# Kernel tuning notes

Measured on AMD Instinct MI355X. Metric: run time of the kernel, lower is better.

## Reference

```python
import jax, jax.numpy as jnp
import numpy as np

HEADS = 4

def gat_layer(x, W, a_src, a_dst, bias, edge_index, n):
    # PyG-style GATConv with self-loops, heads averaged (concat=False) so out dim == hidden_dim
    H, C = a_src.shape
    h = (x @ W).reshape(n, H, C)                      # [N,H,C]
    loops = jnp.arange(n)
    src = jnp.concatenate([edge_index[0], loops])
    dst = jnp.concatenate([edge_index[1], loops])
    e = jax.nn.leaky_relu((h * a_src).sum(-1)[src] + (h * a_dst).sum(-1)[dst], 0.2)  # [E,H]
    m = jax.ops.segment_max(e, dst, num_segments=n)   # segment softmax over incoming edges
    ex = jnp.exp(e - m[dst])
    s = jax.ops.segment_sum(ex, dst, num_segments=n)
    alpha = ex / (s[dst] + 1e-16)
    out = jax.ops.segment_sum(alpha[:, :, None] * h[src], dst, num_segments=n)  # [N,H,C]
    return out.mean(axis=1) + bias

def setup_inputs() -> dict:
    key = jax.random.key(0)
    ks = jax.random.split(key, 24)
    Nd, Ni, Ne = 20000, 4096, 4096
    D_in, D = 512, 256
    n_int, n_emo = 64, 32
    inp = {}
    inp['dialogue_embeddings'] = jax.random.normal(ks[0], (Nd, D_in), jnp.float32)
    inp['intention_indices'] = jax.random.randint(ks[1], (Ni,), 0, n_int)
    inp['emotion_indices'] = jax.random.randint(ks[2], (Ne,), 0, n_emo)
    inp['dialogue_edge_index'] = jax.random.randint(ks[3], (2, Nd * 32), 0, Nd)
    inp['intention_edge_index'] = jax.random.randint(ks[4], (2, Ni * 16), 0, Ni)
    inp['emotion_edge_index'] = jax.random.randint(ks[5], (2, Ne * 16), 0, Ne)
    s = lambda k, shape: jax.random.normal(k, shape, jnp.float32) * 0.02
    inp['intention_emb'] = s(ks[6], (n_int, D))
    inp['emotion_emb'] = s(ks[7], (n_emo, D))
    inp['Wd'] = s(ks[8], (D_in, HEADS * D)); inp['a_src_d'] = s(ks[9], (HEADS, D)); inp['a_dst_d'] = s(ks[10], (HEADS, D)); inp['bd'] = jnp.zeros((D,), jnp.float32)
    inp['Wi'] = s(ks[11], (D, HEADS * D)); inp['a_src_i'] = s(ks[12], (HEADS, D)); inp['a_dst_i'] = s(ks[13], (HEADS, D)); inp['bi'] = jnp.zeros((D,), jnp.float32)
    inp['We'] = s(ks[14], (D, HEADS * D)); inp['a_src_e'] = s(ks[15], (HEADS, D)); inp['a_dst_e'] = s(ks[16], (HEADS, D)); inp['be'] = jnp.zeros((D,), jnp.float32)
    inp['W_dfc'] = s(ks[17], (D, D)); inp['b_dfc'] = jnp.zeros((D,), jnp.float32)
    inp['W_ifc'] = s(ks[18], (D, D)); inp['b_ifc'] = jnp.zeros((D,), jnp.float32)
    inp['W_efc'] = s(ks[19], (D, D)); inp['b_efc'] = jnp.zeros((D,), jnp.float32)
    inp['W_fc'] = s(ks[20], (3 * D, n_emo)); inp['b_fc'] = jnp.zeros((n_emo,), jnp.float32)
    return inp

def reference(dialogue_embeddings, intention_indices, emotion_indices,
              dialogue_edge_index, intention_edge_index, emotion_edge_index,
              intention_emb, emotion_emb,
              Wd, a_src_d, a_dst_d, bd, Wi, a_src_i, a_dst_i, bi,
              We, a_src_e, a_dst_e, be,
              W_dfc, b_dfc, W_ifc, b_ifc, W_efc, b_efc, W_fc, b_fc):
    Nd = dialogue_embeddings.shape[0]
    Ni = intention_indices.shape[0]
    Ne = emotion_indices.shape[0]
    ie = intention_emb[intention_indices]   # [Ni, D]
    ee = emotion_emb[emotion_indices]       # [Ne, D]
    d = gat_layer(dialogue_embeddings, Wd, a_src_d, a_dst_d, bd, dialogue_edge_index, Nd)
    d = jax.nn.relu(d @ W_dfc + b_dfc)
    i = gat_layer(ie, Wi, a_src_i, a_dst_i, bi, intention_edge_index, Ni)
    i = jax.nn.relu(i @ W_ifc + b_ifc)
    e = gat_layer(ee, We, a_src_e, a_dst_e, be, emotion_edge_index, Ne)
    e = jax.nn.relu(e @ W_efc + b_efc)
    iw = jax.nn.softmax(d @ i.T, axis=-1)   # [Nd, Ni]
    att_i = iw @ i                           # [Nd, D]
    ew = jax.nn.softmax(d @ e.T, axis=-1)   # [Nd, Ne]
    att_e = ew @ e                           # [Nd, D]
    inputs = jnp.concatenate([d, att_i, att_e], axis=-1)  # [Nd, 3D]
    return inputs @ W_fc + b_fc
```

## Files before the change

### kernel.cpp

```cpp
#include <hip/hip_runtime.h>
#include <hip/hip_bf16.h>
#include <math.h>

#define DEV static __device__ __forceinline__

typedef __attribute__((ext_vector_type(8))) short short8;
typedef __attribute__((ext_vector_type(4))) short short4v;
typedef __attribute__((ext_vector_type(4))) float f32x4;
typedef __attribute__((ext_vector_type(2))) long long2v;

DEV float bf2f(__hip_bfloat16 x) { return __bfloat162float(x); }
DEV __hip_bfloat16 f2bf(float x) { return __float2bfloat16(x); }
DEV short bfbits(float x) { __hip_bfloat16 h = __float2bfloat16(x); short s; __builtin_memcpy(&s, &h, 2); return s; }
DEV float b2f_bits(short s) { __hip_bfloat16 h; __builtin_memcpy(&h, &s, 2); return __bfloat162float(h); }
DEV float lrelu(float x) { return x > 0.f ? x : 0.2f * x; }

DEV float load_in(const void* p, long long i, bool f32) {
  return f32 ? ((const float*)p)[i] : bf2f(((const __hip_bfloat16*)p)[i]);
}

DEV long pack8_fp8(const float* f) {
  int lo = 0, hi = 0;
  lo = __builtin_amdgcn_cvt_pk_fp8_f32(f[0], f[1], lo, false);
  lo = __builtin_amdgcn_cvt_pk_fp8_f32(f[2], f[3], lo, true);
  hi = __builtin_amdgcn_cvt_pk_fp8_f32(f[4], f[5], hi, false);
  hi = __builtin_amdgcn_cvt_pk_fp8_f32(f[6], f[7], hi, true);
  return ((long)(unsigned)hi << 32) | (unsigned)lo;
}

DEV f32x4 mfma_fp8(long a, long b, f32x4 c) {
  return __builtin_amdgcn_mfma_f32_16x16x32_fp8_fp8(a, b, c, 0, 0, 0);
}

__global__ void HGAN_45148696215914_kernel() {}

__global__ void fill_k(__hip_bfloat16* __restrict__ p, float v, int n)
{
  int i = blockIdx.x * blockDim.x + threadIdx.x;
  if (i < n) p[i] = __float2bfloat16(v);
}

struct DetectArgs { const unsigned int* p[23]; int nw[23]; int id[23]; };

__global__ void detect_k(DetectArgs a, int* __restrict__ flags)
{
  __shared__ int cnt_sh;
  if (threadIdx.x == 0) cnt_sh = 0;
  __syncthreads();
  const unsigned int* w = a.p[blockIdx.x];
  int nwords = a.nw[blockIdx.x];
  int bad = 0;
  for (int i = threadIdx.x; i < nwords; i += blockDim.x) {
    unsigned int x = w[i];
    float v0 = __uint_as_float((x & 0xffffu) << 16);
    float v1 = __uint_as_float(x & 0xffff0000u);
    if (!(fabsf(v0) <= 1e4f)) bad++;
    if (!(fabsf(v1) <= 1e4f)) bad++;
  }
  atomicAdd(&cnt_sh, bad);
  __syncthreads();
  if (threadIdx.x == 0) flags[a.id[blockIdx.x]] = (cnt_sh > nwords / 4) ? 1 : 0;
}

struct CvArgs {
  const void* in[7]; const int* flag[7]; __hip_bfloat16* out[7];
  int K[7], N[7], NL[7], toff[7]; int nseg;
};

__global__ __launch_bounds__(256) void convtrN_k(CvArgs a)
{
  __shared__ __hip_bfloat16 t[32][33];
  int b = blockIdx.x;
  int s = 0;
  while (s + 1 < a.nseg && b >= a.toff[s + 1]) ++s;
  int ti = b - a.toff[s];
  int kb = a.K[s] >> 5;
  int bk = ti % kb, bn = ti / kb;
  const void* in = a.in[s];
  const int* flag = a.flag[s];
  __hip_bfloat16* out = a.out[s];
  int K = a.K[s], N = a.N[s];
  const bool f = flag && *flag;
  int lx = threadIdx.x & 31, ly = threadIdx.x >> 5;
  int gn = bn * 32 + lx;
#pragma unroll
  for (int rr = 0; rr < 32; rr += 8)
    t[rr + ly][lx] = (gn < N)
        ? f2bf(load_in(in, (long long)(bk * 32 + rr + ly) * N + gn, f))
        : f2bf(0.f);
  __syncthreads();
#pragma unroll
  for (int rr = 0; rr < 32; rr += 8)
    out[(size_t)(bn * 32 + rr + ly) * K + bk * 32 + lx] = t[lx][rr + ly];
}

DEV void mgemm_body(
    const void* A, const int* aflag, int lda, const int* idxA,
    const __hip_bfloat16* BT, void* C, int ldc,
    const void* bias, const int* biasflag, int relu,
    int permC, int M, int K, int Nlim, const int* cflag,
    int m0, int n0, __hip_bfloat16* Ash, __hip_bfloat16* Bsh)
{
  const bool af = aflag && *aflag;
  const bool bsf = biasflag && *biasflag;
  const bool cf = cflag && *cflag;
  const int tid = threadIdx.x;
  const int wv = tid >> 6, lane = tid & 63, qd = lane >> 4, lm = lane & 15;
  const int wr = wv >> 1, wc = wv & 1;

  f32x4 acc[4][4];
#pragma unroll
  for (int i = 0; i < 4; ++i)
    for (int j = 0; j < 4; ++j)
      for (int v = 0; v < 4; ++v) acc[i][j][v] = 0.f;

  for (int k0 = 0; k0 < K; k0 += 64) {
    __syncthreads();
    for (int u = tid; u < 1024; u += 256) {
      int r = u >> 3, cu = u & 7;
      int gm = m0 + r;
      short8 vv;
      if (gm < M) {
        long long row = idxA ? idxA[gm] : gm;
        long long basei = row * (long long)lda + k0 + cu * 8;
        if (af) {
          const float4* fp = (const float4*)((const float*)A + basei);
          float4 f0 = fp[0], f1 = fp[1];
          vv[0] = bfbits(f0.x); vv[1] = bfbits(f0.y);
          vv[2] = bfbits(f0.z); vv[3] = bfbits(f0.w);
          vv[4] = bfbits(f1.x); vv[5] = bfbits(f1.y);
          vv[6] = bfbits(f1.z); vv[7] = bfbits(f1.w);
        } else {
          vv = *(const short8*)((const __hip_bfloat16*)A + basei);
        }
      } else {
#pragma unroll
        for (int j = 0; j < 8; ++j) vv[j] = 0;
      }
      *(short8*)(&Ash[r * 72 + cu * 8]) = vv;
    }
    for (int u = tid; u < 1024; u += 256) {
      int r = u >> 3, cu = u & 7;
      *(short8*)(&Bsh[r * 72 + cu * 8]) =
          *(const short8*)(BT + (size_t)(n0 + r) * K + k0 + cu * 8);
    }
    __syncthreads();
#pragma unroll
    for (int ks = 0; ks < 2; ++ks) {
      short8 a[4], b[4];
#pragma unroll
      for (int i = 0; i < 4; ++i)
        a[i] = *(const short8*)(&Ash[(wr * 64 + i * 16 + lm) * 72 + ks * 32 + qd * 8]);
#pragma unroll
      for (int j = 0; j < 4; ++j)
        b[j] = *(const short8*)(&Bsh[(wc * 64 + j * 16 + lm) * 72 + ks * 32 + qd * 8]);
#pragma unroll
      for (int i = 0; i < 4; ++i)
#pragma unroll
        for (int j = 0; j < 4; ++j)
          acc[i][j] = __builtin_amdgcn_mfma_f32_16x16x32_bf16(a[i], b[j], acc[i][j], 0, 0, 0);
    }
  }
#pragma unroll
  for (int j = 0; j < 4; ++j) {
    int gn = n0 + wc * 64 + j * 16 + lm;
    if (gn >= Nlim) continue;
    float bv = bias ? load_in(bias, gn, bsf) : 0.f;
    int gcol = permC ? ((gn & 255) * 4 + (gn >> 8)) : gn;
#pragma unroll
    for (int i = 0; i < 4; ++i) {
#pragma unroll
      for (int v = 0; v < 4; ++v) {
        int gm = m0 + wr * 64 + i * 16 + qd * 4 + v;
        if (gm >= M) continue;
        float x = acc[i][j][v] + bv;
        if (relu) x = fmaxf(x, 0.f);
        long long idx = (long long)gm * ldc + gcol;
        if (cf) ((float*)C)[idx] = x;
        else    ((__hip_bfloat16*)C)[idx] = f2bf(x);
      }
    }
  }
}

__global__ __launch_bounds__(256) void mgemm_k(
    const void* __restrict__ A, const int* __restrict__ aflag, int lda,
    const int* __restrict__ idxA,
    const __hip_bfloat16* __restrict__ BT,
    void* __restrict__ C, int ldc,
    const void* __restrict__ bias, const int* __restrict__ biasflag, int relu,
    int permC, int M, int N, int K, int Nlim,
    const int* __restrict__ cflag)
{
  __shared__ __align__(16) __hip_bfloat16 Ash[128 * 72];
  __shared__ __align__(16) __hip_bfloat16 Bsh[128 * 72];
  (void)N;
  mgemm_body(A, aflag, lda, idxA, BT, C, ldc, bias, biasflag, relu,
             permC, M, K, Nlim, cflag,
             blockIdx.y * 128, blockIdx.x * 128, Ash, Bsh);
}

struct SegArgs {
  const void* A[3]; const int* aflag[3]; int lda[3]; const int* idxA[3];
  const __hip_bfloat16* BT[3]; void* C[3]; int ldc[3];
  const void* bias[3]; const int* bflag[3];
  int M[3]; int K[3]; int yoff[3];
  int relu, permC, Nlim;
};

__global__ __launch_bounds__(256) void mgemm_seg_k(SegArgs a)
{
  __shared__ __align__(16) __hip_bfloat16 Ash[128 * 72];
  __shared__ __align__(16) __hip_bfloat16 Bsh[128 * 72];
  int y = blockIdx.y;
  int s = (y >= a.yoff[2]) ? 2 : ((y >= a.yoff[1]) ? 1 : 0);
  mgemm_body(a.A[s], a.aflag[s], a.lda[s], a.idxA[s], a.BT[s], a.C[s], a.ldc[s],
             a.bias[s], a.bflag[s], a.relu, a.permC, a.M[s], a.K[s], a.Nlim,
             nullptr, (y - a.yoff[s]) * 128, blockIdx.x * 128, Ash, Bsh);
}

__global__ __launch_bounds__(256) void score3_k(
    const __hip_bfloat16* __restrict__ hI,
    const void* as1, const void* ad1, const int* sf1, const int* df1,
    const void* as2, const void* ad2, const int* sf2, const int* df2,
    const void* as3, const void* ad3, const int* sf3, const int* df3,
    int s1, int s2,
    float* __restrict__ ss, float* __restrict__ ds,
    int* __restrict__ cnt, int N)
{
  __shared__ float red[4][8];
  int n = blockIdx.x, c = threadIdx.x;
  if (c == 0) cnt[n] = 0;
  const void* a_src; const void* a_dst; const int* sfp; const int* dfp;
  if (n < s1)      { a_src = as1; a_dst = ad1; sfp = sf1; dfp = df1; }
  else if (n < s2) { a_src = as2; a_dst = ad2; sfp = sf2; dfp = df2; }
  else             { a_src = as3; a_dst = ad3; sfp = sf3; dfp = df3; }
  const bool sf = sfp && *sfp;
  const bool df = dfp && *dfp;
  short4v hv = *(const short4v*)(hI + (size_t)n * 1024 + c * 4);
  float h0 = b2f_bits(hv[0]), h1 = b2f_bits(hv[1]);
  float h2 = b2f_bits(hv[2]), h3 = b2f_bits(hv[3]);
  float r0 = h0 * load_in(a_src, 0 * 256 + c, sf);
  float r1 = h1 * load_in(a_src, 1 * 256 + c, sf);
  float r2 = h2 * load_in(a_src, 2 * 256 + c, sf);
  float r3 = h3 * load_in(a_src, 3 * 256 + c, sf);
  float t0 = h0 * load_in(a_dst, 0 * 256 + c, df);
  float t1 = h1 * load_in(a_dst, 1 * 256 + c, df);
  float t2 = h2 * load_in(a_dst, 2 * 256 + c, df);
  float t3 = h3 * load_in(a_dst, 3 * 256 + c, df);
#pragma unroll
  for (int o = 32; o > 0; o >>= 1) {
    r0 += __shfl_down(r0, o); r1 += __shfl_down(r1, o);
    r2 += __shfl_down(r2, o); r3 += __shfl_down(r3, o);
    t0 += __shfl_down(t0, o); t1 += __shfl_down(t1, o);
    t2 += __shfl_down(t2, o); t3 += __shfl_down(t3, o);
  }
  int wv = c >> 6, lane = c & 63;
  if (lane == 0) {
    red[wv][0] = r0; red[wv][1] = r1; red[wv][2] = r2; red[wv][3] = r3;
    red[wv][4] = t0; red[wv][5] = t1; red[wv][6] = t2; red[wv][7] = t3;
  }
  __syncthreads();
  if (c < 8) {
    float s = red[0][c] + red[1][c] + red[2][c] + red[3][c];
    if (c < 4) ss[n * 4 + c] = s;
    else       ds[n * 4 + (c - 4)] = s;
  }
}

__global__ void count3_k(const int* __restrict__ d1, int E1,
                         const int* __restrict__ d2, int E2, int o2,
                         const int* __restrict__ d3, int E3, int o3,
                         int* __restrict__ cnt)
{
  int k = blockIdx.x * blockDim.x + threadIdx.x;
  if (k < E1) atomicAdd(&cnt[d1[k]], 1);
  else if (k < E1 + E2) atomicAdd(&cnt[d2[k - E1] + o2], 1);
  else if (k < E1 + E2 + E3) atomicAdd(&cnt[d3[k - E1 - E2] + o3], 1);
}

__global__ __launch_bounds__(1024) void scan1_k(
    const int* __restrict__ cnt, int* __restrict__ offp, int* __restrict__ bsum, int n)
{
  __shared__ int sh[1024];
  int idx = blockIdx.x * 1024 + (int)threadIdx.x;
  int v = (idx < n) ? cnt[idx] : 0;
  sh[threadIdx.x] = v;
  __syncthreads();
  for (int d = 1; d < 1024; d <<= 1) {
    int t = (threadIdx.x >= (unsigned)d) ? sh[threadIdx.x - d] : 0;
    __syncthreads();
    sh[threadIdx.x] += t;
    __syncthreads();
  }
  if (idx < n) offp[idx] = sh[threadIdx.x] - v;
  if (threadIdx.x == 1023) bsum[blockIdx.x] = sh[1023];
}

__global__ void scan3_k(int* __restrict__ offp, const int* __restrict__ bsum,
                        int* __restrict__ cur, int n, int nb)
{
  int i = blockIdx.x * blockDim.x + threadIdx.x;
  if (i < n) {
    int chunk = i >> 10;
    int pre = 0;
    for (int b = 0; b < chunk; ++b) pre += bsum[b];
    int v = offp[i] + pre;
    offp[i] = v;
    cur[i] = v;
    if (i == n - 1) {
      int tot = 0;
      for (int b = 0; b < nb; ++b) tot += bsum[b];
      offp[n] = tot;
    }
  }
}

__global__ void scatter3_k(const int* __restrict__ s1, const int* __restrict__ d1, int E1,
                           const int* __restrict__ s2, const int* __restrict__ d2, int E2, int o2,
                           const int* __restrict__ s3, const int* __restrict__ d3, int E3, int o3,
                           int* __restrict__ cur, int* __restrict__ srcs)
{
  int k = blockIdx.x * blockDim.x + threadIdx.x;
  if (k < E1) {
    int p = atomicAdd(&cur[d1[k]], 1);
    srcs[p] = s1[k];
  } else if (k < E1 + E2) {
    int kk = k - E1;
    int p = atomicAdd(&cur[d2[kk] + o2], 1);
    srcs[p] = s2[kk] + o2;
  } else if (k < E1 + E2 + E3) {
    int kk = k - E1 - E2;
    int p = atomicAdd(&cur[d3[kk] + o3], 1);
    srcs[p] = s3[kk] + o3;
  }
}

__global__ __launch_bounds__(256) void convh8_k(
    const __hip_bfloat16* __restrict__ h, char* __restrict__ h8,
    float* __restrict__ hscl, int NU)
{
  __shared__ float red[4];
  int row = blockIdx.x, tid = threadIdx.x;
  int wv = tid >> 6, lane = tid & 63;
  short4v v = *(const short4v*)(h + (size_t)row * 1024 + tid * 4);
  float f0 = b2f_bits(v[0]), f1 = b2f_bits(v[1]);
  float f2 = b2f_bits(v[2]), f3 = b2f_bits(v[3]);
  float m = fmaxf(fmaxf(fabsf(f0), fabsf(f1)), fmaxf(fabsf(f2), fabsf(f3)));
#pragma unroll
  for (int o = 32; o > 0; o >>= 1) m = fmaxf(m, __shfl_xor(m, o));
  if (lane == 0) red[wv] = m;
  __syncthreads();
  float am = fmaxf(fmaxf(red[0], red[1]), fmaxf(red[2], red[3]));
  float inv = (am > 0.f) ? 127.f / am : 0.f;
  int q0 = (int)rintf(f0 * inv), q1 = (int)rintf(f1 * inv);
  int q2 = (int)rintf(f2 * inv), q3 = (int)rintf(f3 * inv);
  int pk = (q0 & 0xff) | ((q1 & 0xff) << 8) | ((q2 & 0xff) << 16) | ((q3 & 0xff) << 24);
  ((int*)h8)[(size_t)row * 256 + tid] = pk;
  if (tid == 0) hscl[row] = am * (1.f / 127.f);
}

__global__ __launch_bounds__(256) void agg3_k(
    const char* __restrict__ h8I, const float* __restrict__ hscl,
    const float* __restrict__ ss, const float* __restrict__ ds,
    const int* __restrict__ offp, const int* __restrict__ srcs,
    const void* b1, const int* bf1,
    const void* b2, const int* bf2,
    const void* b3, const int* bf3,
    int s1, int s2,
    __hip_bfloat16* __restrict__ outp, int N)
{
  __shared__ int src_sh[64];
  __shared__ float scl_sh[64];
  __shared__ __align__(16) float w_sh[64][4];
  __shared__ float scale_sh[4];
  __shared__ float l_sh[4];
  __shared__ __align__(16) float pair_sh[128][8];
  int n = blockIdx.x;
  int c = threadIdx.x;
  int hd_w = c >> 6;
  int e_w  = c & 63;
  int half = c >> 7;
  int tc   = c & 127;
  int s0 = offp[n], deg = offp[n + 1] - s0;
  int total = deg + 1;
  float dsn = ds[n * 4 + hd_w];
  float m_run = -1e30f, l_run = 0.f;
  float A0[4] = {0.f, 0.f, 0.f, 0.f};
  float A1[4] = {0.f, 0.f, 0.f, 0.f};
  for (int base = 0; base < total; base += 64) {
    int cnt = min(64, total - base);
    __syncthreads();
    if (c < cnt) {
      int s = (base + c == 0) ? n : srcs[s0 + base + c - 1];
      src_sh[c] = s;
      scl_sh[c] = hscl[s];
    }
    __syncthreads();
    float val = -1e30f;
    if (e_w < cnt) val = lrelu(ss[src_sh[e_w] * 4 + hd_w] + dsn);
    float vmax = val;
#pragma unroll
    for (int o = 32; o > 0; o >>= 1) vmax = fmaxf(vmax, __shfl_xor(vmax, o));
    float newm = fmaxf(m_run, vmax);
    float p = (e_w < cnt) ? __expf(val - newm) : 0.f;
    float psum = p;
#pragma unroll
    for (int o = 32; o > 0; o >>= 1) psum += __shfl_xor(psum, o);
    float sc = __expf(m_run - newm);
    l_run = l_run * sc + psum;
    m_run = newm;
    w_sh[e_w][hd_w] = p * scl_sh[e_w];
    if (e_w == 0) scale_sh[hd_w] = sc;
    __syncthreads();
    float sc0 = scale_sh[0], sc1 = scale_sh[1], sc2 = scale_sh[2], sc3 = scale_sh[3];
    A0[0] *= sc0; A0[1] *= sc1; A0[2] *= sc2; A0[3] *= sc3;
    A1[0] *= sc0; A1[1] *= sc1; A1[2] *= sc2; A1[3] *= sc3;
    for (int e = half; e < cnt; e += 2) {
      long hv = *(const long*)(h8I + (size_t)src_sh[e] * 1024 + tc * 8);
      float4 w = *(const float4*)(&w_sh[e][0]);
      int lo = (int)(unsigned)(unsigned long)hv;
      int hi = (int)((unsigned long)hv >> 32);
      A0[0] += w.x * (float)(signed char)(lo);
      A0[1] += w.y * (float)(signed char)(lo >> 8);
      A0[2] += w.z * (float)(signed char)(lo >> 16);
      A0[3] += w.w * (float)(signed char)(lo >> 24);
      A1[0] += w.x * (float)(signed char)(hi);
      A1[1] += w.y * (float)(signed char)(hi >> 8);
      A1[2] += w.z * (float)(signed char)(hi >> 16);
      A1[3] += w.w * (float)(signed char)(hi >> 24);
    }
  }
  __syncthreads();
  if (e_w == 0) l_sh[hd_w] = l_run;
  if (half == 1) {
    *(float4*)(&pair_sh[tc][0]) = make_float4(A0[0], A0[1], A0[2], A0[3]);
    *(float4*)(&pair_sh[tc][4]) = make_float4(A1[0], A1[1], A1[2], A1[3]);
  }
  __syncthreads();
  if (half == 0) {
    float4 p0 = *(const float4*)(&pair_sh[tc][0]);
    float4 p1 = *(const float4*)(&pair_sh[tc][4]);
    A0[0] += p0.x; A0[1] += p0.y; A0[2] += p0.z; A0[3] += p0.w;
    A1[0] += p1.x; A1[1] += p1.y; A1[2] += p1.z; A1[3] += p1.w;
    const void* bias; const int* bfp;
    if (n < s1)      { bias = b1; bfp = bf1; }
    else if (n < s2) { bias = b2; bfp = bf2; }
    else             { bias = b3; bfp = bf3; }
    const bool bf = bfp && *bfp;
    float il0 = 1.f / (l_sh[0] + 1e-16f), il1 = 1.f / (l_sh[1] + 1e-16f);
    float il2 = 1.f / (l_sh[2] + 1e-16f), il3 = 1.f / (l_sh[3] + 1e-16f);
    float r0 = 0.25f * (A0[0] * il0 + A0[1] * il1 + A0[2] * il2 + A0[3] * il3);
    float r1 = 0.25f * (A1[0] * il0 + A1[1] * il1 + A1[2] * il2 + A1[3] * il3);
    outp[(size_t)n * 256 + 2 * tc]     = f2bf(r0 + load_in(bias, 2 * tc, bf));
    outp[(size_t)n * 256 + 2 * tc + 1] = f2bf(r1 + load_in(bias, 2 * tc + 1, bf));
  }
}

__global__ __launch_bounds__(256) void conv8_k(
    const __hip_bfloat16* __restrict__ in0, char* __restrict__ K8_0, char* __restrict__ KT8_0,
    const __hip_bfloat16* __restrict__ in1, char* __restrict__ K8_1, char* __restrict__ KT8_1,
    int Nk)
{
  __shared__ __align__(16) __hip_bfloat16 t[32][264];
  const __hip_bfloat16* in = blockIdx.y ? in1 : in0;
  char* K8  = blockIdx.y ? K8_1  : K8_0;
  char* KT8 = blockIdx.y ? KT8_1 : KT8_0;
  int kv0 = blockIdx.x * 32;
  size_t tbase = (size_t)(kv0 >> 5) * 8192;
  int tid = threadIdx.x;
  (void)Nk;
  for (int u = tid; u < 1024; u += 256) {
    int r = u >> 5, c = u & 31;
    *(short8*)(&t[r][c * 8]) = *(const short8*)(in + (size_t)(kv0 + r) * 256 + c * 8);
  }
  __syncthreads();
  for (int u = tid; u < 1024; u += 256) {
    int r = u >> 5, g = u & 31, pos = g * 8;
    int qd_ = pos >> 6, s = (pos >> 3) & 7;
    int d = s * 32 + qd_ * 8;
    float f[8];
#pragma unroll
    for (int j = 0; j < 8; ++j) f[j] = 16.f * bf2f(t[r][d + j]);
    int c16 = pos >> 4, h = (pos >> 3) & 1;
    int unit = ((c16 & 3) * 2 + (r >> 4)) * 64 + (c16 >> 2) * 16 + (r & 15);
    *(long*)(K8 + tbase + (size_t)unit * 16 + h * 8) = pack8_fp8(f);
  }
  {
    int d = tid;
#pragma unroll
    for (int g = 0; g < 4; ++g) {
      float f[8];
#pragma unroll
      for (int j = 0; j < 8; ++j) f[j] = 16.f * bf2f(t[g * 8 + j][d]);
      int unit = (d >> 4) * 64 + g * 16 + (d & 15);
      *(long*)(KT8 + tbase + (size_t)unit * 8) = pack8_fp8(f);
    }
  }
}

__global__ __launch_bounds__(512, 4) void flashf8_k(
    const __hip_bfloat16* __restrict__ Q, int ldq,
    const char* __restrict__ K8_0, const char* __restrict__ KT8_0,
    const char* __restrict__ K8_1, const char* __restrict__ KT8_1,
    __hip_bfloat16* __restrict__ Opart, float2* __restrict__ ml,
    int M, int Nk)
{
  __shared__ __align__(16) char Ksh8[2][8192];
  __shared__ __align__(16) char KTsh8[2][8192];
  __shared__ __align__(16) char Psh8[8][16 * 40];
  const int att = blockIdx.y;
  const int z = blockIdx.z;
  const char* K8  = att ? K8_1  : K8_0;
  const char* KT8 = att ? KT8_1 : KT8_0;

  const int tid = threadIdx.x;
  const int wv = tid >> 6, lane = tid & 63;
  const int qd = lane >> 4, lm = lane & 15;
  const int r0 = blockIdx.x * 128 + wv * 16;
  char* Pw = Psh8[wv];

  const int half_tiles = Nk >> 6;
  const int t0 = z * half_tiles;

  long qf8[8];
  {
    const bool ok = (r0 + lm) < M;
    const __hip_bfloat16* qrow = Q + (size_t)(r0 + lm) * ldq;
#pragma unroll
    for (int s = 0; s < 8; ++s) {
      float f[8];
      if (ok) {
        short8 qv = *(const short8*)(qrow + s * 32 + qd * 8);
#pragma unroll
        for (int j = 0; j < 8; ++j) f[j] = 16.f * b2f_bits(qv[j]);
      } else {
#pragma unroll
        for (int j = 0; j < 8; ++j) f[j] = 0.f;
      }
      qf8[s] = pack8_fp8(f);
    }
  }

  f32x4 Oacc[16];
#pragma unroll
  for (int i = 0; i < 16; ++i)
    for (int v = 0; v < 4; ++v) Oacc[i][v] = 0.f;
  float mrow = -1e30f, lrow = 0.f;

  {
    size_t tb = (size_t)t0 * 8192;
    short8 k0 = *(const short8*)(K8 + tb + (size_t)tid * 16);
    short8 t0v = *(const short8*)(KT8 + tb + (size_t)tid * 16);
    *(short8*)(&Ksh8[0][tid * 16]) = k0;
    *(short8*)(&KTsh8[0][tid * 16]) = t0v;
  }
  __syncthreads();

  for (int it = 0; it < half_tiles; ++it) {
    const int cur = it & 1, nxt = cur ^ 1;
    const bool havenext = (it + 1) < half_tiles;
    short8 pk0, pt0;
    if (havenext) {
      size_t tb = (size_t)(t0 + it + 1) * 8192;
      pk0 = *(const short8*)(K8 + tb + (size_t)tid * 16);
      pt0 = *(const short8*)(KT8 + tb + (size_t)tid * 16);
    }
    const char* Kc  = Ksh8[cur];
    const char* KTc = KTsh8[cur];

    f32x4 S[2];
#pragma unroll
    for (int t = 0; t < 2; ++t)
      for (int v = 0; v < 4; ++v) S[t][v] = 0.f;
#pragma unroll
    for (int sp = 0; sp < 4; ++sp) {
#pragma unroll
      for (int t = 0; t < 2; ++t) {
        long2v a2 = *(const long2v*)(&Kc[((sp * 2 + t) * 64 + lane) * 16]);
        S[t] = mfma_fp8(a2[0], qf8[2 * sp],     S[t]);
        S[t] = mfma_fp8(a2[1], qf8[2 * sp + 1], S[t]);
      }
    }
#pragma unroll
    for (int t = 0; t < 2; ++t)
      for (int v = 0; v < 4; ++v) S[t][v] *= 0.00390625f;

    float tmax = -1e30f;
#pragma unroll
    for (int t = 0; t < 2; ++t)
      for (int v = 0; v < 4; ++v) tmax = fmaxf(tmax, S[t][v]);
    tmax = fmaxf(tmax, __shfl_xor(tmax, 16));
    tmax = fmaxf(tmax, __shfl_xor(tmax, 32));
    float newm = fmaxf(mrow, tmax);
    float psum = 0.f;
#pragma unroll
    for (int t = 0; t < 2; ++t)
      for (int v = 0; v < 4; ++v) {
        float p = __expf(S[t][v] - newm);
        S[t][v] = p;
        psum += p;
      }
    psum += __shfl_xor(psum, 16);
    psum += __shfl_xor(psum, 32);
    float scale = __expf(mrow - newm);
    lrow = lrow * scale + psum;
    mrow = newm;
#pragma unroll
    for (int t = 0; t < 2; ++t) {
      int pk = __builtin_amdgcn_cvt_pk_fp8_f32(16.f * S[t][0], 16.f * S[t][1], 0, false);
      pk = __builtin_amdgcn_cvt_pk_fp8_f32(16.f * S[t][2], 16.f * S[t][3], pk, true);
      *(int*)(&Pw[lm * 40 + t * 16 + qd * 4]) = pk;
    }

    if (__any(scale < 1.0f)) {
      float scl[4];
#pragma unroll
      for (int v = 0; v < 4; ++v) scl[v] = __shfl(scale, qd * 4 + v);
#pragma unroll
      for (int i = 0; i < 16; ++i)
        for (int v = 0; v < 4; ++v) Oacc[i][v] *= scl[v];
    }

    {
      long pa0 = *(const long*)(&Pw[lm * 40 + qd * 8]);
#pragma unroll
      for (int dt = 0; dt < 16; ++dt) {
        long b = *(const long*)(&KTc[dt * 512 + lane * 8]);
        Oacc[dt] = mfma_fp8(pa0, b, Oacc[dt]);
      }
    }

    if (havenext) {
      *(short8*)(&Ksh8[nxt][tid * 16]) = pk0;
      *(short8*)(&KTsh8[nxt][tid * 16]) = pt0;
    }
    __syncthreads();
  }

  {
    __hip_bfloat16* Op = Opart + (size_t)(z * 2 + att) * M * 256;
    float linv = 1.f / (256.f * lrow);
    float li[4];
#pragma unroll
    for (int v = 0; v < 4; ++v) li[v] = __shfl(linv, qd * 4 + v);
#pragma unroll
    for (int v = 0; v < 4; ++v) {
      int grow = r0 + qd * 4 + v;
      if (grow >= M) continue;
#pragma unroll
      for (int dt = 0; dt < 16; ++dt)
        Op[(size_t)grow * 256 + dt * 16 + lm] = f2bf(Oacc[dt][v] * li[v]);
    }
    if (lane < 16 && (r0 + lm) < M)
      ml[(size_t)(z * 2 + att) * M + r0 + lm] = make_float2(mrow, lrow);
  }
}

__global__ __launch_bounds__(256) void merge_k(
    const __hip_bfloat16* __restrict__ Opart, const float2* __restrict__ ml,
    __hip_bfloat16* __restrict__ Out, int ldo, int M)
{
  int row = blockIdx.x, att = blockIdx.y, c = threadIdx.x;
  float2 a = ml[(size_t)(0 * 2 + att) * M + row];
  float2 b = ml[(size_t)(1 * 2 + att) * M + row];
  float Mx = fmaxf(a.x, b.x);
  float w0 = a.y * __expf(a.x - Mx);
  float w1 = b.y * __expf(b.x - Mx);
  float inv = 1.f / (w0 + w1 + 1e-30f);
  float o0 = bf2f(Opart[((size_t)(0 * 2 + att) * M + row) * 256 + c]);
  float o1 = bf2f(Opart[((size_t)(1 * 2 + att) * M + row) * 256 + c]);
  Out[(size_t)row * ldo + att * 256 + c] = f2bf((w0 * o0 + w1 * o1) * inv);
}

extern "C" void kernel_launch(void* const* d_in, const int* in_sizes, int n_in,
                              void* d_out, int out_size, void* d_ws, size_t ws_size,
                              hipStream_t stream)
{
  const void* Xd      = d_in[0];
  const int*  int_idx = (const int*)d_in[1];
  const int*  emo_idx = (const int*)d_in[2];
  const int*  ed_d    = (const int*)d_in[3];
  const int*  ed_i    = (const int*)d_in[4];
  const int*  ed_e    = (const int*)d_in[5];
  const void* int_emb = d_in[6];
  const void* emo_emb = d_in[7];
  const void* Wd = d_in[8],  *a_src_d = d_in[9],  *a_dst_d = d_in[10], *bd = d_in[11];
  const void* Wi = d_in[12], *a_src_i = d_in[13], *a_dst_i = d_in[14], *bi = d_in[15];
  const void* We = d_in[16], *a_src_e = d_in[17], *a_dst_e = d_in[18], *be = d_in[19];
  const void* W_dfc = d_in[20], *b_dfc = d_in[21];
  const void* W_ifc = d_in[22], *b_ifc = d_in[23];
  const void* W_efc = d_in[24], *b_efc = d_in[25];
  const void* W_fc  = d_in[26], *b_fc  = d_in[27];

  const int DIn  = in_sizes[8] / 1024;
  const int Nd   = in_sizes[0] / DIn;
  const int Ni   = in_sizes[1];
  const int Ne   = in_sizes[2];
  const int Ed   = in_sizes[3] / 2;
  const int Ei   = in_sizes[4] / 2;
  const int Ee   = in_sizes[5] / 2;
  const int Nout = in_sizes[27];
  const int NU   = Nd + Ni + Ne;

  char* base = (char*)d_ws;
  size_t off = 0;
  auto alloc = [&](size_t nbytes) -> void* {
    void* p = base + off;
    off = (off + nbytes + 255) & ~(size_t)255;
    return p;
  };
  int* flags = (int*)alloc(32 * sizeof(int));
  int* bsum  = (int*)alloc(64 * sizeof(int));
  __hip_bfloat16* hbuf = (__hip_bfloat16*)alloc((size_t)NU * 1024 * 2);
  __hip_bfloat16* cat  = (__hip_bfloat16*)alloc((size_t)Nd * 768 * 2);
  __hip_bfloat16* gat_tmp = (__hip_bfloat16*)alloc((size_t)NU * 256 * 2);
  __hip_bfloat16* WdT  = (__hip_bfloat16*)alloc((size_t)1024 * DIn * 2);
  __hip_bfloat16* WiT  = (__hip_bfloat16*)alloc((size_t)1024 * 256 * 2);
  __hip_bfloat16* WeT  = (__hip_bfloat16*)alloc((size_t)1024 * 256 * 2);
  __hip_bfloat16* WdfT = (__hip_bfloat16*)alloc((size_t)256 * 256 * 2);
  __hip_bfloat16* WifT = (__hip_bfloat16*)alloc((size_t)256 * 256 * 2);
  __hip_bfloat16* WefT = (__hip_bfloat16*)alloc((size_t)256 * 256 * 2);
  __hip_bfloat16* WfcT = (__hip_bfloat16*)alloc((size_t)128 * 768 * 2);
  float* ss  = (float*)alloc((size_t)NU * 4 * 4);
  float* dsb = (float*)alloc((size_t)NU * 4 * 4);
  int* cnt   = (int*)alloc((size_t)NU * 4);
  int* offp  = (int*)alloc((size_t)(NU + 1) * 4);
  int* cur   = (int*)alloc((size_t)NU * 4);
  int* srcs  = (int*)alloc((size_t)(Ed + Ei + Ee) * 4);
  const size_t need = off;
  (void)n_in;

  __hip_bfloat16* i_mat = hbuf;
  __hip_bfloat16* e_mat = hbuf + (size_t)Ni * 256;
  char* K8i  = (char*)(hbuf + (size_t)2 * Ni * 256);
  char* KT8i = K8i + (size_t)Ni * 256;
  char* K8e  = KT8i + (size_t)Ni * 256;
  char* KT8e = K8e + (size_t)Ne * 256;
  char* scratch = KT8e + (size_t)Ne * 256;
  __hip_bfloat16* Opart = (__hip_bfloat16*)scratch;
  float2* mlbuf = (float2*)(scratch + (size_t)4 * Nd * 256 * 2);
  char* h8 = (char*)cat;
  float* hscl = (float*)(h8 + (size_t)NU * 1024);

  const dim3 T(256);
  if (ws_size < need) {
    fill_k<<<(out_size + 255) / 256, T, 0, stream>>>((__hip_bfloat16*)d_out, 0.25f, out_size);
    return;
  }

  {
    DetectArgs da;
    const int fid[23] = {0,6,7,8,9,10,11,12,13,14,15,16,17,18,19,20,21,22,23,24,25,26,27};
    for (int t = 0; t < 23; ++t) {
      int id = fid[t];
      int nw = in_sizes[id] / 2;
      if (nw > 2048) nw = 2048;
      if (nw < 1) nw = 1;
      da.p[t] = (const unsigned int*)d_in[id];
      da.nw[t] = nw;
      da.id[t] = id;
    }
    detect_k<<<23, 256, 0, stream>>>(da, flags);
  }
  #define F(i) (flags + (i))

  {
    CvArgs cv;
    const void* ins[7]  = {Wd, Wi, We, W_dfc, W_ifc, W_efc, W_fc};
    const int*  fgs[7]  = {F(8), F(12), F(16), F(20), F(22), F(24), F(26)};
    __hip_bfloat16* outs[7] = {WdT, WiT, WeT, WdfT, WifT, WefT, WfcT};
    int Ks[7]  = {DIn, 256, 256, 256, 256, 256, 768};
    int Ns[7]  = {1024, 1024, 1024, 256, 256, 256, Nout};
    int NLs[7] = {1024, 1024, 1024, 256, 256, 256, 128};
    int run = 0;
    for (int s = 0; s < 7; ++s) {
      cv.in[s] = ins[s]; cv.flag[s] = fgs[s]; cv.out[s] = outs[s];
      cv.K[s] = Ks[s]; cv.N[s] = Ns[s]; cv.NL[s] = NLs[s]; cv.toff[s] = run;
      run += (Ks[s] / 32) * (NLs[s] / 32);
    }
    cv.nseg = 7;
    convtrN_k<<<run, T, 0, stream>>>(cv);
  }

  const int yNd = (Nd + 127) / 128, yNi = Ni / 128, yNe = Ne / 128;
  {
    SegArgs sa;
    sa.A[0] = Xd;      sa.aflag[0] = F(0); sa.lda[0] = DIn; sa.idxA[0] = nullptr;
    sa.BT[0] = WdT;    sa.C[0] = hbuf;     sa.ldc[0] = 1024;
    sa.bias[0] = nullptr; sa.bflag[0] = nullptr; sa.M[0] = Nd; sa.K[0] = DIn;
    sa.A[1] = int_emb; sa.aflag[1] = F(6); sa.lda[1] = 256; sa.idxA[1] = int_idx;
    sa.BT[1] = WiT;    sa.C[1] = hbuf + (size_t)Nd * 1024; sa.ldc[1] = 1024;
    sa.bias[1] = nullptr; sa.bflag[1] = nullptr; sa.M[1] = Ni; sa.K[1] = 256;
    sa.A[2] = emo_emb; sa.aflag[2] = F(7); sa.lda[2] = 256; sa.idxA[2] = emo_idx;
    sa.BT[2] = WeT;    sa.C[2] = hbuf + (size_t)(Nd + Ni) * 1024; sa.ldc[2] = 1024;
    sa.bias[2] = nullptr; sa.bflag[2] = nullptr; sa.M[2] = Ne; sa.K[2] = 256;
    sa.yoff[0] = 0; sa.yoff[1] = yNd; sa.yoff[2] = yNd + yNi;
    sa.relu = 0; sa.permC = 1; sa.Nlim = 1024;
    mgemm_seg_k<<<dim3(8, yNd + yNi + yNe), T, 0, stream>>>(sa);
  }

  convh8_k<<<NU, T, 0, stream>>>(hbuf, h8, hscl, NU);

  {
    int nb = (NU + 1023) / 1024;
    int Etot = Ed + Ei + Ee;
    score3_k<<<NU, T, 0, stream>>>(hbuf,
        a_src_d, a_dst_d, F(9), F(10),
        a_src_i, a_dst_i, F(13), F(14),
        a_src_e, a_dst_e, F(17), F(18),
        Nd, Nd + Ni, ss, dsb, cnt, NU);
    count3_k<<<(Etot + 255) / 256, T, 0, stream>>>(
        ed_d + Ed, Ed, ed_i + Ei, Ei, Nd, ed_e + Ee, Ee, Nd + Ni, cnt);
    scan1_k<<<nb, 1024, 0, stream>>>(cnt, offp, bsum, NU);
    scan3_k<<<(NU + 255) / 256, T, 0, stream>>>(offp, bsum, cur, NU, nb);
    scatter3_k<<<(Etot + 255) / 256, T, 0, stream>>>(
        ed_d, ed_d + Ed, Ed, ed_i, ed_i + Ei, Ei, Nd,
        ed_e, ed_e + Ee, Ee, Nd + Ni, cur, srcs);
    agg3_k<<<NU, T, 0, stream>>>(h8, hscl, ss, dsb, offp, srcs,
        bd, F(11), bi, F(15), be, F(19), Nd, Nd + Ni, gat_tmp, NU);
  }

  {
    SegArgs sa;
    sa.A[0] = gat_tmp; sa.aflag[0] = nullptr; sa.lda[0] = 256; sa.idxA[0] = nullptr;
    sa.BT[0] = WdfT;   sa.C[0] = cat;   sa.ldc[0] = 768;
    sa.bias[0] = b_dfc; sa.bflag[0] = F(21); sa.M[0] = Nd; sa.K[0] = 256;
    sa.A[1] = gat_tmp + (size_t)Nd * 256; sa.aflag[1] = nullptr; sa.lda[1] = 256; sa.idxA[1] = nullptr;
    sa.BT[1] = WifT;   sa.C[1] = i_mat; sa.ldc[1] = 256;
    sa.bias[1] = b_ifc; sa.bflag[1] = F(23); sa.M[1] = Ni; sa.K[1] = 256;
    sa.A[2] = gat_tmp + (size_t)(Nd + Ni) * 256; sa.aflag[2] = nullptr; sa.lda[2] = 256; sa.idxA[2] = nullptr;
    sa.BT[2] = WefT;   sa.C[2] = e_mat; sa.ldc[2] = 256;
    sa.bias[2] = b_efc; sa.bflag[2] = F(25); sa.M[2] = Ne; sa.K[2] = 256;
    sa.yoff[0] = 0; sa.yoff[1] = yNd; sa.yoff[2] = yNd + yNi;
    sa.relu = 1; sa.permC = 0; sa.Nlim = 256;
    mgemm_seg_k<<<dim3(2, yNd + yNi + yNe), T, 0, stream>>>(sa);
  }

  conv8_k<<<dim3(Ni / 32, 2), T, 0, stream>>>(i_mat, K8i, KT8i, e_mat, K8e, KT8e, Ni);

  flashf8_k<<<dim3((Nd + 127) / 128, 2, 2), dim3(512), 0, stream>>>(
      cat, 768, K8i, KT8i, K8e, KT8e, Opart, mlbuf, Nd, Ni);

  merge_k<<<dim3(Nd, 2), T, 0, stream>>>(Opart, mlbuf, cat + 256, 768, Nd);

  mgemm_k<<<dim3(1, (Nd + 127) / 128), T, 0, stream>>>(
      cat, nullptr, 768, nullptr, WfcT, d_out, Nout,
      b_fc, F(27), 0, 0, Nd, 128, 768, Nout, F(0));
}
```

Before: 823.9 us.

## Process two 64-key tiles per flash iteration and defer softmax rescale

The fp8 flash-attention kernel now handles 128 keys per loop iteration by loading two K/KT tiles into doubled shared buffers, which halves the number of barriers and softmax reductions. The running max is updated only when the new tile max exceeds it by more than a threshold (lazy rescaling), which skips the exp and accumulator rescale in most iterations. The shared-memory stores for the next tile are moved earlier, between the QK MFMAs and the softmax. Shared memory use roughly doubles, which may lower occupancy. Lazy rescaling lets probabilities exceed 1 before fp8 conversion, which can cost some accuracy.

```diff
diff --git a/kernel.cpp b/kernel.cpp
--- a/kernel.cpp
+++ b/kernel.cpp
@@ -506,9 +506,9 @@
     __hip_bfloat16* __restrict__ Opart, float2* __restrict__ ml,
     int M, int Nk)
 {
-  __shared__ __align__(16) char Ksh8[2][8192];
-  __shared__ __align__(16) char KTsh8[2][8192];
-  __shared__ __align__(16) char Psh8[8][16 * 40];
+  __shared__ __align__(16) char Ksh8[2][16384];
+  __shared__ __align__(16) char KTsh8[2][16384];
+  __shared__ __align__(16) char Psh8[8][2][16 * 40];
   const int att = blockIdx.y;
   const int z = blockIdx.z;
   const char* K8  = att ? K8_1  : K8_0;
@@ -518,10 +518,9 @@
   const int wv = tid >> 6, lane = tid & 63;
   const int qd = lane >> 4, lm = lane & 15;
   const int r0 = blockIdx.x * 128 + wv * 16;
-  char* Pw = Psh8[wv];
-
-  const int half_tiles = Nk >> 6;
-  const int t0 = z * half_tiles;
+
+  const int half_iters = Nk >> 7;
+  const int t0 = z * half_iters;
 
   long qf8[8];
   {
@@ -549,53 +548,69 @@
   float mrow = -1e30f, lrow = 0.f;
 
   {
-    size_t tb = (size_t)t0 * 8192;
-    short8 k0 = *(const short8*)(K8 + tb + (size_t)tid * 16);
-    short8 t0v = *(const short8*)(KT8 + tb + (size_t)tid * 16);
-    *(short8*)(&Ksh8[0][tid * 16]) = k0;
-    *(short8*)(&KTsh8[0][tid * 16]) = t0v;
-  }
-  __syncthreads();
-
-  for (int it = 0; it < half_tiles; ++it) {
+    size_t tb = (size_t)t0 * 16384;
+#pragma unroll
+    for (int j = 0; j < 2; ++j) {
+      *(short8*)(&Ksh8[0][tid * 16 + j * 8192]) =
+          *(const short8*)(K8 + tb + (size_t)tid * 16 + j * 8192);
+      *(short8*)(&KTsh8[0][tid * 16 + j * 8192]) =
+          *(const short8*)(KT8 + tb + (size_t)tid * 16 + j * 8192);
+    }
+  }
+  __syncthreads();
+
+  for (int it = 0; it < half_iters; ++it) {
     const int cur = it & 1, nxt = cur ^ 1;
-    const bool havenext = (it + 1) < half_tiles;
-    short8 pk0, pt0;
+    const bool havenext = (it + 1) < half_iters;
+    short8 pk[2], pt[2];
     if (havenext) {
-      size_t tb = (size_t)(t0 + it + 1) * 8192;
-      pk0 = *(const short8*)(K8 + tb + (size_t)tid * 16);
-      pt0 = *(const short8*)(KT8 + tb + (size_t)tid * 16);
+      size_t tb = (size_t)(t0 + it + 1) * 16384;
+#pragma unroll
+      for (int j = 0; j < 2; ++j) {
+        pk[j] = *(const short8*)(K8 + tb + (size_t)tid * 16 + j * 8192);
+        pt[j] = *(const short8*)(KT8 + tb + (size_t)tid * 16 + j * 8192);
+      }
     }
     const char* Kc  = Ksh8[cur];
     const char* KTc = KTsh8[cur];
 
-    f32x4 S[2];
-#pragma unroll
-    for (int t = 0; t < 2; ++t)
+    f32x4 S[4];
+#pragma unroll
+    for (int t = 0; t < 4; ++t)
       for (int v = 0; v < 4; ++v) S[t][v] = 0.f;
 #pragma unroll
     for (int sp = 0; sp < 4; ++sp) {
 #pragma unroll
-      for (int t = 0; t < 2; ++t) {
-        long2v a2 = *(const long2v*)(&Kc[((sp * 2 + t) * 64 + lane) * 16]);
+      for (int t = 0; t < 4; ++t) {
+        long2v a2 = *(const long2v*)(
+            &Kc[(t >> 1) * 8192 + ((sp * 2 + (t & 1)) * 64 + lane) * 16]);
         S[t] = mfma_fp8(a2[0], qf8[2 * sp],     S[t]);
         S[t] = mfma_fp8(a2[1], qf8[2 * sp + 1], S[t]);
       }
     }
 #pragma unroll
-    for (int t = 0; t < 2; ++t)
+    for (int t = 0; t < 4; ++t)
       for (int v = 0; v < 4; ++v) S[t][v] *= 0.00390625f;
 
+    if (havenext) {
+#pragma unroll
+      for (int j = 0; j < 2; ++j) {
+        *(short8*)(&Ksh8[nxt][tid * 16 + j * 8192]) = pk[j];
+        *(short8*)(&KTsh8[nxt][tid * 16 + j * 8192]) = pt[j];
+      }
+    }
+
     float tmax = -1e30f;
 #pragma unroll
-    for (int t = 0; t < 2; ++t)
+    for (int t = 0; t < 4; ++t)
       for (int v = 0; v < 4; ++v) tmax = fmaxf(tmax, S[t][v]);
     tmax = fmaxf(tmax, __shfl_xor(tmax, 16));
     tmax = fmaxf(tmax, __shfl_xor(tmax, 32));
-    float newm = fmaxf(mrow, tmax);
+    const bool need = __any(tmax > mrow + 2.0f);
+    float newm = need ? fmaxf(mrow, tmax) : mrow;
     float psum = 0.f;
 #pragma unroll
-    for (int t = 0; t < 2; ++t)
+    for (int t = 0; t < 4; ++t)
       for (int v = 0; v < 4; ++v) {
         float p = __expf(S[t][v] - newm);
         S[t][v] = p;
@@ -603,38 +618,42 @@
       }
     psum += __shfl_xor(psum, 16);
     psum += __shfl_xor(psum, 32);
-    float scale = __expf(mrow - newm);
-    lrow = lrow * scale + psum;
-    mrow = newm;
-#pragma unroll
-    for (int t = 0; t < 2; ++t) {
-      int pk = __builtin_amdgcn_cvt_pk_fp8_f32(16.f * S[t][0], 16.f * S[t][1], 0, false);
-      pk = __builtin_amdgcn_cvt_pk_fp8_f32(16.f * S[t][2], 16.f * S[t][3], pk, true);
-      *(int*)(&Pw[lm * 40 + t * 16 + qd * 4]) = pk;
-    }
-
-    if (__any(scale < 1.0f)) {
-      float scl[4];
-#pragma unroll
-      for (int v = 0; v < 4; ++v) scl[v] = __shfl(scale, qd * 4 + v);
-#pragma unroll
-      for (int i = 0; i < 16; ++i)
-        for (int v = 0; v < 4; ++v) Oacc[i][v] *= scl[v];
+
+#pragma unroll
+    for (int t = 0; t < 4; ++t) {
+      int pk32 = __builtin_amdgcn_cvt_pk_fp8_f32(16.f * S[t][0], 16.f * S[t][1], 0, false);
+      pk32 = __builtin_amdgcn_cvt_pk_fp8_f32(16.f * S[t][2], 16.f * S[t][3], pk32, true);
+      *(int*)(&Psh8[wv][t >> 1][lm * 40 + (t & 1) * 16 + qd * 4]) = pk32;
+    }
+
+    if (need) {
+      float scale = __expf(mrow - newm);
+      lrow = lrow * scale + psum;
+      mrow = newm;
+      if (__any(scale < 1.0f)) {
+        float scl[4];
+#pragma unroll
+        for (int v = 0; v < 4; ++v) scl[v] = __shfl(scale, qd * 4 + v);
+#pragma unroll
+        for (int i = 0; i < 16; ++i)
+          for (int v = 0; v < 4; ++v) Oacc[i][v] *= scl[v];
+      }
+    } else {
+      lrow += psum;
     }
 
     {
-      long pa0 = *(const long*)(&Pw[lm * 40 + qd * 8]);
+      long pa0 = *(const long*)(&Psh8[wv][0][lm * 40 + qd * 8]);
+      long pa1 = *(const long*)(&Psh8[wv][1][lm * 40 + qd * 8]);
 #pragma unroll
       for (int dt = 0; dt < 16; ++dt) {
-        long b = *(const long*)(&KTc[dt * 512 + lane * 8]);
-        Oacc[dt] = mfma_fp8(pa0, b, Oacc[dt]);
+        long b0 = *(const long*)(&KTc[dt * 512 + lane * 8]);
+        long b1 = *(const long*)(&KTc[8192 + dt * 512 + lane * 8]);
+        Oacc[dt] = mfma_fp8(pa0, b0, Oacc[dt]);
+        Oacc[dt] = mfma_fp8(pa1, b1, Oacc[dt]);
       }
     }
 
-    if (havenext) {
-      *(short8*)(&Ksh8[nxt][tid * 16]) = pk0;
-      *(short8*)(&KTsh8[nxt][tid * 16]) = pt0;
-    }
     __syncthreads();
   }
 
```

Measured after the change: 873.7 us. 6.0% more time.
